# Optimization experiments

Hardware: AMD Instinct MI355X
Metric: run time of the kernel (lower is better)

Reference implementation:

```python
import jax, jax.numpy as jnp
import numpy as np
import math

D = 1024
H = 8
HD = D // H
TEMP = math.sqrt(D)
EPS = 1e-5

def _layernorm(x, g, b):
    mu = jnp.mean(x, axis=-1, keepdims=True)
    var = jnp.var(x, axis=-1, keepdims=True)
    return (x - mu) * jax.lax.rsqrt(var + EPS) * g + b

def setup_inputs() -> dict:
    key = jax.random.key(0)
    ks = jax.random.split(key, 8)
    B, Lq, Lk = 4, 2048, 2048
    Q = jax.random.normal(ks[0], (B, Lq, D), dtype=jnp.float32)
    K = jax.random.normal(ks[1], (B, Lk, D), dtype=jnp.float32)
    V = jax.random.normal(ks[2], (B, Lk, D), dtype=jnp.float32)
    Wq = jax.random.normal(ks[3], (D, D), dtype=jnp.float32) * 0.02
    Wk = jax.random.normal(ks[4], (D, D), dtype=jnp.float32) * 0.02
    Wv = jax.random.normal(ks[5], (D, D), dtype=jnp.float32) * 0.02
    Wo = jax.random.normal(ks[6], (D, D), dtype=jnp.float32) * 0.02
    pre_g = jnp.ones((D,), jnp.float32)
    pre_b = jnp.zeros((D,), jnp.float32)
    ln_g = jnp.ones((D,), jnp.float32)
    ln_b = jnp.zeros((D,), jnp.float32)
    return {"Q": Q, "K": K, "V": V, "Wq": Wq, "Wk": Wk, "Wv": Wv, "Wo": Wo,
            "pre_g": pre_g, "pre_b": pre_b, "ln_g": ln_g, "ln_b": ln_b}

def reference(Q, K, V, Wq, Wk, Wv, Wo, pre_g, pre_b, ln_g, ln_b):
    B, Lq, _ = Q.shape
    Lk = K.shape[1]
    # pre-LN on Q and K only (V untouched, as in original)
    Qn = _layernorm(Q, pre_g, pre_b)
    Kn = _layernorm(K, pre_g, pre_b)
    q = (Qn @ Wq).reshape(B, Lq, H, HD)
    k = (Kn @ Wk).reshape(B, Lk, H, HD)
    v = (V @ Wv).reshape(B, Lk, H, HD)
    scores = jnp.einsum('bqhd,bkhd->bhqk', q, k) / TEMP
    scores = jnp.clip(scores, -10000.0, 10000.0)
    A = jax.nn.softmax(scores, axis=-1)  # dropout = identity in eval
    O = jnp.einsum('bhqk,bkhd->bqhd', A, v).reshape(B, Lq, D)
    O = _layernorm(O, ln_g, ln_b)
    O = O + jax.nn.gelu(O @ Wo, approximate=False)  # residual branch
    return O
```

## Files before the change

### kernel.cpp

```cpp
#include <hip/hip_runtime.h>
#include <math.h>

typedef unsigned short u16;
typedef __bf16 bf16x8 __attribute__((ext_vector_type(8)));
typedef float f32x4 __attribute__((ext_vector_type(4)));

union B8u { uint4 u; bf16x8 v; u16 s[8]; };

__device__ __forceinline__ u16 f2bf(float f){
  unsigned u = __float_as_uint(f);
  u += 0x7fffu + ((u >> 16) & 1u);
  return (u16)(u >> 16);
}
__device__ __forceinline__ bf16x8 ld8(const u16* p){
  B8u x; x.u = *(const uint4*)p; return x.v;
}
__device__ __forceinline__ void glds16(const u16* g, u16* l){
  __builtin_amdgcn_global_load_lds(
      (const __attribute__((address_space(1))) void*)g,
      (__attribute__((address_space(3))) void*)l, 16, 0, 0);
}

__global__ void wcast_k(const float* __restrict__ Wq, const float* __restrict__ Wk,
                        const float* __restrict__ Wv, const float* __restrict__ Wo,
                        u16* __restrict__ Tq, u16* __restrict__ Tk,
                        u16* __restrict__ Tv, u16* __restrict__ To){
  const float* W; u16* T;
  switch(blockIdx.z){
    case 0: W = Wq; T = Tq; break;
    case 1: W = Wk; T = Tk; break;
    case 2: W = Wv; T = Tv; break;
    default: W = Wo; T = To; break;
  }
  __shared__ u16 tile[32][33];
  int tx = threadIdx.x & 31, ty = threadIdx.x >> 5;
  int n0 = blockIdx.x * 32, k0 = blockIdx.y * 32;
  for(int i = ty; i < 32; i += 8)
    tile[i][tx] = f2bf(W[(size_t)(k0 + i) * 1024 + n0 + tx]);
  __syncthreads();
  for(int i = ty; i < 32; i += 8)
    T[(size_t)(n0 + i) * 1024 + k0 + tx] = tile[tx][i];
}

__global__ void ln_cast(const float* __restrict__ X, u16* __restrict__ Y,
                        float* __restrict__ Yf,
                        const float* __restrict__ g, const float* __restrict__ bb,
                        int doLN){
  __shared__ float red[8];
  int row = blockIdx.x;
  int t = threadIdx.x;
  float4 v = ((const float4*)(X + (size_t)row * 1024))[t];
  float o0 = v.x, o1 = v.y, o2 = v.z, o3 = v.w;
  if(doLN){
    float s  = o0 + o1 + o2 + o3;
    float ss = o0*o0 + o1*o1 + o2*o2 + o3*o3;
    for(int o = 32; o > 0; o >>= 1){
      s  += __shfl_down(s,  o, 64);
      ss += __shfl_down(ss, o, 64);
    }
    if((t & 63) == 0){ red[t >> 6] = s; red[4 + (t >> 6)] = ss; }
    __syncthreads();
    s  = red[0] + red[1] + red[2] + red[3];
    ss = red[4] + red[5] + red[6] + red[7];
    float mu  = s * (1.f/1024.f);
    float var = ss * (1.f/1024.f) - mu*mu;
    float rs  = rsqrtf(var + 1e-5f);
    float4 gg = ((const float4*)g)[t];
    float4 bv = ((const float4*)bb)[t];
    o0 = (o0 - mu) * rs * gg.x + bv.x;
    o1 = (o1 - mu) * rs * gg.y + bv.y;
    o2 = (o2 - mu) * rs * gg.z + bv.z;
    o3 = (o3 - mu) * rs * gg.w + bv.w;
  }
  if(Yf){
    float4 w; w.x=o0; w.y=o1; w.z=o2; w.w=o3;
    ((float4*)(Yf + (size_t)row * 1024))[t] = w;
  }
  ushort4 u;
  u.x = f2bf(o0); u.y = f2bf(o1); u.z = f2bf(o2); u.w = f2bf(o3);
  ((ushort4*)(Y + (size_t)row * 1024))[t] = u;
}

template<int MODE>
__global__ __launch_bounds__(256,2) void gemm_bt(
  const u16* __restrict__ A, const u16* __restrict__ Bt,
  u16* __restrict__ Obf, float* __restrict__ Of32, const float* __restrict__ Resid,
  int ldC, float oscale)
{
  __shared__ u16 as[128*64];
  __shared__ u16 bs[128*64];
  const int K = 1024;
  int t = threadIdx.x;
  int wave = t >> 6, lane = t & 63, quad = lane >> 4, l16 = lane & 15;
  int m0 = blockIdx.x * 128, n0 = blockIdx.y * 128;
  int wm = (wave >> 1) * 64, wn = (wave & 1) * 64;
  int srow = t >> 3;
  f32x4 acc[4][4] = {};
  for(int k0 = 0; k0 < K; k0 += 64){
    __syncthreads();
    for(int p = 0; p < 4; p++){
      int r = p*32 + srow;
      int c = (t & 7) ^ (r & 7);
      glds16(A  + (size_t)(m0 + r) * K + k0 + c*8, as + p*2048 + wave*512);
      glds16(Bt + (size_t)(n0 + r) * K + k0 + c*8, bs + p*2048 + wave*512);
    }
    __syncthreads();
    bf16x8 af[2][4], bfr[2][4];
    for(int kk = 0; kk < 2; kk++)
      for(int mt = 0; mt < 4; mt++){
        int ra = wm + mt*16 + l16;
        af[kk][mt]  = ld8(&as[ra*64 + (((kk*4 + quad) ^ (ra & 7)) * 8)]);
        int rb = wn + mt*16 + l16;
        bfr[kk][mt] = ld8(&bs[rb*64 + (((kk*4 + quad) ^ (rb & 7)) * 8)]);
      }
    for(int kk = 0; kk < 2; kk++)
      for(int mt = 0; mt < 4; mt++)
        for(int nt = 0; nt < 4; nt++)
          acc[mt][nt] = __builtin_amdgcn_mfma_f32_16x16x32_bf16(af[kk][mt], bfr[kk][nt], acc[mt][nt], 0, 0, 0);
  }
  for(int mt = 0; mt < 4; mt++)
    for(int nt = 0; nt < 4; nt++){
      int col = n0 + wn + nt*16 + l16;
      for(int r = 0; r < 4; r++){
        int row = m0 + wm + mt*16 + quad*4 + r;
        size_t idx = (size_t)row * ldC + col;
        float v = acc[mt][nt][r];
        if(MODE == 0){
          Obf[idx] = f2bf(v * oscale);
        } else {
          float ge = 0.5f * v * (1.0f + erff(v * 0.70710678118f));
          Of32[idx] = Resid[idx] + ge;
        }
      }
    }
}

__global__ __launch_bounds__(256,3) void flash_k(
  const u16* __restrict__ Qp, const u16* __restrict__ Kp, const u16* __restrict__ VT,
  float* __restrict__ Oout)
{
  __shared__ u16 ks[64*128];
  __shared__ u16 vts[128*64];
  __shared__ u16 ps[64][72];
  int t = threadIdx.x, wave = t >> 6, lane = t & 63, quad = lane >> 4, l16 = lane & 15;
  int l = blockIdx.x;
  int xcd = l & 7, i = l >> 3;
  int bh = xcd + 8 * (i & 3);
  int qt = i >> 2;
  int b = bh >> 3, h = bh & 7;
  size_t rowbase = (size_t)b * 2048;
  int colbase = h * 128;
  int wq = wave * 16;

  bf16x8 aq[4];
  {
    const u16* qrow = Qp + (rowbase + qt*64 + wq + l16) * 1024 + colbase + quad*8;
    for(int kk = 0; kk < 4; kk++) aq[kk] = ld8(qrow + kk*32);
  }

  float l_i[4] = {0.f, 0.f, 0.f, 0.f};
  f32x4 oacc[8] = {};

  int krow = t >> 4;
  int kchunk = lane & 15;
  int vrow = t >> 3;
  int vchunk = lane & 7;

  for(int kt = 0; kt < 2048; kt += 64){
    __syncthreads();
    for(int p = 0; p < 4; p++){
      int kr = p*16 + krow;
      int ck = kchunk ^ (kr & 15);
      glds16(Kp + (rowbase + kt + kr) * 1024 + colbase + ck*8,
             ks + p*2048 + wave*512);
      int vr = p*32 + vrow;
      int cv = vchunk ^ (vr & 7);
      glds16(VT + (size_t)(colbase + vr) * 8192 + rowbase + kt + cv*8,
             vts + p*2048 + wave*512);
    }
    __syncthreads();

    f32x4 s[4];
    for(int ct = 0; ct < 4; ct++){
      f32x4 accS = {};
      for(int kk = 0; kk < 4; kk++){
        bf16x8 bb = ld8(&ks[(ct*16 + l16)*128 + (((kk*4 + quad) ^ l16) * 8)]);
        accS = __builtin_amdgcn_mfma_f32_16x16x32_bf16(aq[kk], bb, accS, 0, 0, 0);
      }
      s[ct] = accS;
    }
    for(int ct = 0; ct < 4; ct++)
      for(int r = 0; r < 4; r++){
        float p = __expf(fminf(s[ct][r], 80.f));
        s[ct][r] = p;
      }
    for(int r = 0; r < 4; r++){
      l_i[r] += (s[0][r] + s[1][r]) + (s[2][r] + s[3][r]);
      for(int ct = 0; ct < 4; ct++) ps[wq + quad*4 + r][ct*16 + l16] = f2bf(s[ct][r]);
    }
    bf16x8 pa0 = ld8(&ps[wq + l16][quad*8]);
    bf16x8 pa1 = ld8(&ps[wq + l16][32 + quad*8]);
    for(int dt = 0; dt < 8; dt++){
      int vrw = (dt*16 + l16)*64;
      int r7 = l16 & 7;
      bf16x8 b0 = ld8(&vts[vrw + ((quad ^ r7) * 8)]);
      oacc[dt] = __builtin_amdgcn_mfma_f32_16x16x32_bf16(pa0, b0, oacc[dt], 0, 0, 0);
      bf16x8 b1 = ld8(&vts[vrw + (((4 + quad) ^ r7) * 8)]);
      oacc[dt] = __builtin_amdgcn_mfma_f32_16x16x32_bf16(pa1, b1, oacc[dt], 0, 0, 0);
    }
  }
  float rinv[4];
  for(int r = 0; r < 4; r++){
    float lv = l_i[r];
    for(int o = 1; o < 16; o <<= 1) lv += __shfl_xor(lv, o, 64);
    rinv[r] = 1.f / lv;
  }
  for(int dt = 0; dt < 8; dt++){
    int col = colbase + dt*16 + l16;
    for(int r = 0; r < 4; r++){
      size_t row = rowbase + qt*64 + wq + quad*4 + r;
      Oout[row * 1024 + col] = oacc[dt][r] * rinv[r];
    }
  }
}

extern "C" void kernel_launch(void* const* d_in, const int* in_sizes, int n_in,
                              void* d_out, int out_size, void* d_ws, size_t ws_size,
                              hipStream_t stream){
  (void)in_sizes; (void)n_in; (void)out_size; (void)ws_size;
  const float* Q    = (const float*)d_in[0];
  const float* K    = (const float*)d_in[1];
  const float* V    = (const float*)d_in[2];
  const float* Wq   = (const float*)d_in[3];
  const float* Wk   = (const float*)d_in[4];
  const float* Wv   = (const float*)d_in[5];
  const float* Wo   = (const float*)d_in[6];
  const float* pre_g = (const float*)d_in[7];
  const float* pre_b = (const float*)d_in[8];
  const float* ln_g  = (const float*)d_in[9];
  const float* ln_b  = (const float*)d_in[10];
  float* Out = (float*)d_out;
  char* ws = (char*)d_ws;
  const size_t MB = 1024 * 1024;
  u16* WTq = (u16*)(ws + 0*MB);
  u16* WTk = (u16*)(ws + 2*MB);
  u16* WTv = (u16*)(ws + 4*MB);
  u16* WTo = (u16*)(ws + 6*MB);
  u16* QN  = (u16*)(ws + 8*MB);
  u16* KN  = (u16*)(ws + 24*MB);
  u16* VB  = (u16*)(ws + 40*MB);
  u16* QP  = (u16*)(ws + 56*MB);
  u16* KP  = (u16*)(ws + 72*MB);
  u16* VT  = (u16*)(ws + 88*MB);
  float* OLN  = (float*)(ws + 8*MB);
  u16*   OLNb = (u16*)(ws + 40*MB);

  wcast_k<<<dim3(32,32,4), 256, 0, stream>>>(Wq,Wk,Wv,Wo, WTq,WTk,WTv,WTo);
  ln_cast<<<8192, 256, 0, stream>>>(Q, QN, nullptr, pre_g, pre_b, 1);
  ln_cast<<<8192, 256, 0, stream>>>(K, KN, nullptr, pre_g, pre_b, 1);
  ln_cast<<<8192, 256, 0, stream>>>(V, VB, nullptr, pre_g, pre_b, 0);
  gemm_bt<0><<<dim3(64,8), 256, 0, stream>>>(QN, WTq, QP, nullptr, nullptr, 1024, 0.03125f);
  gemm_bt<0><<<dim3(64,8), 256, 0, stream>>>(KN, WTk, KP, nullptr, nullptr, 1024, 1.0f);
  gemm_bt<0><<<dim3(8,64), 256, 0, stream>>>(WTv, VB, VT, nullptr, nullptr, 8192, 1.0f);
  flash_k<<<1024, 256, 0, stream>>>(QP, KP, VT, Out);
  ln_cast<<<8192, 256, 0, stream>>>(Out, OLNb, OLN, ln_g, ln_b, 1);
  gemm_bt<1><<<dim3(64,8), 256, 0, stream>>>(OLNb, WTo, nullptr, Out, OLN, 1024, 1.0f);
}
```

Measured before the change: 397.0 us.

## Batch QKV launches into single kernels and use exp2 softmax with folded log2e

Merges the three pre-LN/cast launches into one 3D-grid kernel and the three Q/K/V projection GEMMs into one 1536-block kernel, so the GPU sees fewer, larger launches and the tail of each projection can overlap with the next. In the attention kernel, log2(e) is folded into the Q projection scale so the softmax uses the hardware exp2 instruction directly. The clamp at 80 is dropped, and P is converted to bf16 with a cheaper round-half-up instead of round-to-nearest-even. This trades a little rounding fidelity and overflow protection for fewer ALU ops and less launch overhead.

```diff
diff --git a/kernel.cpp b/kernel.cpp
--- a/kernel.cpp
+++ b/kernel.cpp
@@ -42,13 +42,11 @@
     T[(size_t)(n0 + i) * 1024 + k0 + tx] = tile[tx][i];
 }
 
-__global__ void ln_cast(const float* __restrict__ X, u16* __restrict__ Y,
-                        float* __restrict__ Yf,
-                        const float* __restrict__ g, const float* __restrict__ bb,
-                        int doLN){
-  __shared__ float red[8];
-  int row = blockIdx.x;
-  int t = threadIdx.x;
+__device__ __forceinline__ void ln_core(const float* __restrict__ X,
+                                        u16* __restrict__ Y, float* __restrict__ Yf,
+                                        const float* __restrict__ g,
+                                        const float* __restrict__ bb,
+                                        int doLN, int row, int t, float* red){
   float4 v = ((const float4*)(X + (size_t)row * 1024))[t];
   float o0 = v.x, o1 = v.y, o2 = v.z, o3 = v.w;
   if(doLN){
@@ -81,18 +79,36 @@
   ((ushort4*)(Y + (size_t)row * 1024))[t] = u;
 }
 
+__global__ void ln3_cast(const float* __restrict__ Q, const float* __restrict__ K,
+                         const float* __restrict__ V,
+                         u16* __restrict__ QN, u16* __restrict__ KN, u16* __restrict__ VB,
+                         const float* __restrict__ g, const float* __restrict__ bb){
+  __shared__ float red[8];
+  const float* X; u16* Y; int doLN = 1;
+  switch(blockIdx.y){
+    case 0: X = Q; Y = QN; break;
+    case 1: X = K; Y = KN; break;
+    default: X = V; Y = VB; doLN = 0; break;
+  }
+  ln_core(X, Y, nullptr, g, bb, doLN, blockIdx.x, threadIdx.x, red);
+}
+
+__global__ void ln_post(const float* __restrict__ X, u16* __restrict__ Y,
+                        float* __restrict__ Yf,
+                        const float* __restrict__ g, const float* __restrict__ bb){
+  __shared__ float red[8];
+  ln_core(X, Y, Yf, g, bb, 1, blockIdx.x, threadIdx.x, red);
+}
+
 template<int MODE>
-__global__ __launch_bounds__(256,2) void gemm_bt(
+__device__ __forceinline__ void gemm_core(
   const u16* __restrict__ A, const u16* __restrict__ Bt,
   u16* __restrict__ Obf, float* __restrict__ Of32, const float* __restrict__ Resid,
-  int ldC, float oscale)
+  int m0, int n0, int ldC, float oscale, u16* as, u16* bs)
 {
-  __shared__ u16 as[128*64];
-  __shared__ u16 bs[128*64];
   const int K = 1024;
   int t = threadIdx.x;
   int wave = t >> 6, lane = t & 63, quad = lane >> 4, l16 = lane & 15;
-  int m0 = blockIdx.x * 128, n0 = blockIdx.y * 128;
   int wm = (wave >> 1) * 64, wn = (wave & 1) * 64;
   int srow = t >> 3;
   f32x4 acc[4][4] = {};
@@ -133,6 +149,33 @@
         }
       }
     }
+}
+
+__global__ __launch_bounds__(256,2) void qkv_gemm(
+  const u16* __restrict__ QN, const u16* __restrict__ KN, const u16* __restrict__ VB,
+  const u16* __restrict__ WTq, const u16* __restrict__ WTk, const u16* __restrict__ WTv,
+  u16* __restrict__ QP, u16* __restrict__ KP, u16* __restrict__ VT, float qscale)
+{
+  __shared__ u16 as[128*64];
+  __shared__ u16 bs[128*64];
+  int bx = blockIdx.x;
+  int z = bx % 3, id = bx / 3;
+  if(z == 0){
+    gemm_core<0>(QN, WTq, QP, nullptr, nullptr, (id >> 3)*128, (id & 7)*128, 1024, qscale, as, bs);
+  } else if(z == 1){
+    gemm_core<0>(KN, WTk, KP, nullptr, nullptr, (id >> 3)*128, (id & 7)*128, 1024, 1.0f, as, bs);
+  } else {
+    gemm_core<0>(WTv, VB, VT, nullptr, nullptr, (id & 7)*128, (id >> 3)*128, 8192, 1.0f, as, bs);
+  }
+}
+
+__global__ __launch_bounds__(256,2) void out_gemm(
+  const u16* __restrict__ A, const u16* __restrict__ Bt,
+  float* __restrict__ Of32, const float* __restrict__ Resid)
+{
+  __shared__ u16 as[128*64];
+  __shared__ u16 bs[128*64];
+  gemm_core<1>(A, Bt, nullptr, Of32, Resid, blockIdx.x*128, blockIdx.y*128, 1024, 1.0f, as, bs);
 }
 
 __global__ __launch_bounds__(256,3) void flash_k(
@@ -190,13 +233,14 @@
       s[ct] = accS;
     }
     for(int ct = 0; ct < 4; ct++)
-      for(int r = 0; r < 4; r++){
-        float p = __expf(fminf(s[ct][r], 80.f));
-        s[ct][r] = p;
-      }
+      for(int r = 0; r < 4; r++)
+        s[ct][r] = __builtin_amdgcn_exp2f(s[ct][r]);
     for(int r = 0; r < 4; r++){
       l_i[r] += (s[0][r] + s[1][r]) + (s[2][r] + s[3][r]);
-      for(int ct = 0; ct < 4; ct++) ps[wq + quad*4 + r][ct*16 + l16] = f2bf(s[ct][r]);
+      for(int ct = 0; ct < 4; ct++){
+        unsigned u = __float_as_uint(s[ct][r]) + 0x8000u;
+        ps[wq + quad*4 + r][ct*16 + l16] = (u16)(u >> 16);
+      }
     }
     bf16x8 pa0 = ld8(&ps[wq + l16][quad*8]);
     bf16x8 pa1 = ld8(&ps[wq + l16][32 + quad*8]);
@@ -255,14 +299,12 @@
   float* OLN  = (float*)(ws + 8*MB);
   u16*   OLNb = (u16*)(ws + 40*MB);
 
+  const float qscale = 0.03125f * 1.44269504089f;
+
   wcast_k<<<dim3(32,32,4), 256, 0, stream>>>(Wq,Wk,Wv,Wo, WTq,WTk,WTv,WTo);
-  ln_cast<<<8192, 256, 0, stream>>>(Q, QN, nullptr, pre_g, pre_b, 1);
-  ln_cast<<<8192, 256, 0, stream>>>(K, KN, nullptr, pre_g, pre_b, 1);
-  ln_cast<<<8192, 256, 0, stream>>>(V, VB, nullptr, pre_g, pre_b, 0);
-  gemm_bt<0><<<dim3(64,8), 256, 0, stream>>>(QN, WTq, QP, nullptr, nullptr, 1024, 0.03125f);
-  gemm_bt<0><<<dim3(64,8), 256, 0, stream>>>(KN, WTk, KP, nullptr, nullptr, 1024, 1.0f);
-  gemm_bt<0><<<dim3(8,64), 256, 0, stream>>>(WTv, VB, VT, nullptr, nullptr, 8192, 1.0f);
+  ln3_cast<<<dim3(8192,3), 256, 0, stream>>>(Q, K, V, QN, KN, VB, pre_g, pre_b);
+  qkv_gemm<<<1536, 256, 0, stream>>>(QN, KN, VB, WTq, WTk, WTv, QP, KP, VT, qscale);
   flash_k<<<1024, 256, 0, stream>>>(QP, KP, VT, Out);
-  ln_cast<<<8192, 256, 0, stream>>>(Out, OLNb, OLN, ln_g, ln_b, 1);
-  gemm_bt<1><<<dim3(64,8), 256, 0, stream>>>(OLNb, WTo, nullptr, Out, OLN, 1024, 1.0f);
-}
+  ln_post<<<8192, 256, 0, stream>>>(Out, OLNb, OLN, ln_g, ln_b);
+  out_gemm<<<dim3(64,8), 256, 0, stream>>>(OLNb, WTo, Out, OLN);
+}
```

Measured after the change: 386.0 us. 2.8% less time.
